# Kernel optimization log

Measured on AMD Instinct MI355X. Metric: run time of the kernel, lower is better.

The kernel has to match this reference:

```python
import jax, jax.numpy as jnp
import numpy as np

TOP_K = 8  # num_experts_per_tok
NEG_INF = -1e9


def setup_inputs() -> dict:
    key = jax.random.key(0)
    ks = jax.random.split(key, 6)
    B, S, H, I, E, G, GS = 1, 2048, 2048, 1408, 64, 8, 8
    sc = 0.02
    return {
        "hidden_states": jax.random.normal(ks[0], (B, S, H), jnp.float32),
        "gate_w": jax.random.normal(ks[1], (E, H), jnp.float32) * sc,
        "mask_up_w": jax.random.normal(ks[2], (G, H, GS), jnp.float32) * sc,
        "gate_proj_w": jax.random.normal(ks[3], (G, I, H), jnp.float32) * sc,
        "up_proj_w": jax.random.normal(ks[4], (G, I, H), jnp.float32) * sc,
        "down_proj_w": jax.random.normal(ks[5], (G, H, I), jnp.float32) * sc,
        "inv_map": jnp.arange(G * GS, dtype=jnp.int64).reshape(G, GS),
    }


def reference(hidden_states, gate_w, mask_up_w, gate_proj_w, up_proj_w, down_proj_w, inv_map):
    B, S, H = hidden_states.shape
    x = hidden_states.reshape(-1, H)  # [N, H]
    N = x.shape[0]
    E = gate_w.shape[0]

    # Gate: softmax scores -> top-k routing (DeepSeek-style MoEGate)
    scores = jax.nn.softmax(x @ gate_w.T, axis=-1)          # [N, E]
    topk_w, topk_idx = jax.lax.top_k(scores, TOP_K)         # [N, K]

    # Per-expert routing weight: w_e[t, e] = sum_k topk_w[t,k] * (topk_idx[t,k]==e)
    w_e = jnp.zeros((N, E), x.dtype).at[jnp.arange(N)[:, None], topk_idx].add(topk_w)

    # Gather group-local weights: flat[t, g, i] for sub-expert i of group g
    flat = w_e[:, inv_map]                                   # [N, G, GS]
    scalar = flat.sum(-1)                                    # [N, G]
    soft = jax.nn.softmax(jnp.where(flat == 0, NEG_INF, flat), axis=-1)  # [N, G, GS]

    # Mask injection: x' = x + mask_up_proj(soft)
    xg = x[:, None, :] + jnp.einsum('ngi,ghi->ngh', soft, mask_up_w)     # [N, G, H]

    # SwiGLU per group
    g = jnp.einsum('ngh,gih->ngi', xg, gate_proj_w)          # [N, G, I]
    u = jnp.einsum('ngh,gih->ngi', xg, up_proj_w)            # [N, G, I]
    a = jax.nn.silu(g) * u
    d = jnp.einsum('ngi,ghi->ngh', a, down_proj_w)           # [N, G, H]

    # scalar * output, accumulated over groups (scalar==0 rows contribute 0,
    # matching the original's zero-masked scatter)
    y = jnp.einsum('ng,ngh->nh', scalar, d)
    return y.reshape(B, S, H)
```

## Files before the change

kernel.cpp:

```cpp
#include <hip/hip_runtime.h>

#define N_TOK 2048
#define H_DIM 2048
#define I_DIM 1408
#define E_EXP 64
#define G_GRP 8
#define KTOT  (G_GRP * I_DIM)

typedef __bf16 bf16x8 __attribute__((ext_vector_type(8)));
typedef float f32x4 __attribute__((ext_vector_type(4)));

__device__ __forceinline__ unsigned short f2bf(float f) {
    unsigned int u = __builtin_bit_cast(unsigned int, f);
    u += 0x7fffu + ((u >> 16) & 1u);
    return (unsigned short)(u >> 16);
}

__device__ __forceinline__ float bf2f(unsigned short s) {
    return __builtin_bit_cast(float, (unsigned int)s << 16);
}

__device__ __forceinline__ void gl_lds16(const void* g, void* l) {
    __builtin_amdgcn_global_load_lds(
        (const __attribute__((address_space(1))) unsigned int*)g,
        (__attribute__((address_space(3))) unsigned int*)l, 16, 0, 0);
}

__device__ __forceinline__ bf16x8 lds_frag(const unsigned short* sm, int row, int c) {
    return *(const bf16x8*)&sm[(row * 8 + (c ^ (row & 7))) * 8];
}

__global__ __launch_bounds__(256) void k_transpose(const float* __restrict__ gw,
                                                   float* __restrict__ gwT) {
    int i = blockIdx.x * 256 + threadIdx.x;
    int h = i >> 6, e = i & 63;
    gwT[i] = gw[e * H_DIM + h];
}

__global__ __launch_bounds__(256) void k_cvt(const float* __restrict__ in,
                                             unsigned short* __restrict__ out, int n4) {
    int i = blockIdx.x * 256 + threadIdx.x;
    if (i >= n4) return;
    float4 v = ((const float4*)in)[i];
    ushort4 o;
    o.x = f2bf(v.x); o.y = f2bf(v.y); o.z = f2bf(v.z); o.w = f2bf(v.w);
    ((ushort4*)out)[i] = o;
}

__global__ __launch_bounds__(256) void k_cvt_wd(const float* __restrict__ in,
                                                unsigned short* __restrict__ out) {
    int idx = blockIdx.x * 256 + threadIdx.x;
    int i4 = idx % (I_DIM / 4);
    int h  = (idx / (I_DIM / 4)) & (H_DIM - 1);
    int g  = idx / ((I_DIM / 4) * H_DIM);
    float4 v = ((const float4*)(in + ((size_t)g * H_DIM + h) * I_DIM))[i4];
    ushort4 o;
    o.x = f2bf(v.x); o.y = f2bf(v.y); o.z = f2bf(v.z); o.w = f2bf(v.w);
    ((ushort4*)(out + ((size_t)h * G_GRP + g) * I_DIM))[i4] = o;
}

__global__ __launch_bounds__(512) void k_gating(const float* __restrict__ x,
                                                const float* __restrict__ gwT,
                                                float* __restrict__ soft,
                                                float* __restrict__ scal) {
    __shared__ double smAcc[8][8][64];
    int t = threadIdx.x, wid = t >> 6, lane = t & 63;
    int n0 = blockIdx.x * 8;

    double acc[8];
#pragma unroll
    for (int k = 0; k < 8; ++k) acc[k] = 0.0;
    int h0 = wid * 256;
    for (int h = h0; h < h0 + 256; ++h) {
        float gv = gwT[h * 64 + lane];
#pragma unroll
        for (int tok = 0; tok < 8; ++tok)
            acc[tok] += (double)x[(size_t)(n0 + tok) * H_DIM + h] * (double)gv;
    }
#pragma unroll
    for (int tok = 0; tok < 8; ++tok) smAcc[wid][tok][lane] = acc[tok];
    __syncthreads();

    double lg = 0.0;
#pragma unroll
    for (int w2 = 0; w2 < 8; ++w2) lg += smAcc[w2][wid][lane];
    float logit = (float)lg;

    float mx = logit;
#pragma unroll
    for (int d = 1; d < 64; d <<= 1) mx = fmaxf(mx, __shfl_xor(mx, d));
    float ex = expf(logit - mx);
    float sm = ex;
#pragma unroll
    for (int d = 1; d < 64; d <<= 1) sm += __shfl_xor(sm, d);
    float prob = ex / sm;

    float cur = prob, w = 0.0f;
#pragma unroll
    for (int it = 0; it < 8; ++it) {
        float m = cur;
#pragma unroll
        for (int d = 1; d < 64; d <<= 1) m = fmaxf(m, __shfl_xor(m, d));
        unsigned long long msk = __ballot(cur == m);
        int first = __ffsll(msk) - 1;
        if (lane == first) { w = prob; cur = -1.0f; }
    }
    float wf = w;

    float s8 = wf;
#pragma unroll
    for (int d = 1; d < 8; d <<= 1) s8 += __shfl_xor(s8, d);
    float v = (wf == 0.0f) ? -1000000000.0f : wf;
    float m8 = v;
#pragma unroll
    for (int d = 1; d < 8; d <<= 1) m8 = fmaxf(m8, __shfl_xor(m8, d));
    float e8 = expf(v - m8);
    float q8 = e8;
#pragma unroll
    for (int d = 1; d < 8; d <<= 1) q8 += __shfl_xor(q8, d);

    int n = n0 + wid;
    soft[(size_t)n * 64 + lane] = e8 / q8;
    if ((lane & 7) == 0) scal[(size_t)n * 8 + (lane >> 3)] = s8;
}

__global__ __launch_bounds__(256) void k_xg(const float* __restrict__ x,
                                            const float* __restrict__ muw,
                                            const float* __restrict__ soft,
                                            unsigned short* __restrict__ xg) {
    int g = blockIdx.z, h0 = blockIdx.y * 256, n0 = blockIdx.x * 128;
    __shared__ float smMu[8][256];
    __shared__ float smSf[128][8];
    int t = threadIdx.x;
    {
        const float* p = muw + ((size_t)g * H_DIM + h0 + t) * 8;
#pragma unroll
        for (int s = 0; s < 8; ++s) smMu[s][t] = p[s];
        int r = t >> 1, s4 = (t & 1) * 4;
        float4 sv = *(const float4*)&soft[(size_t)(n0 + r) * 64 + g * 8 + s4];
        smSf[r][s4 + 0] = sv.x; smSf[r][s4 + 1] = sv.y;
        smSf[r][s4 + 2] = sv.z; smSf[r][s4 + 3] = sv.w;
    }
    __syncthreads();
    const float* xp = x + (size_t)n0 * H_DIM + h0 + t;
    unsigned short* op = xg + ((size_t)g * N_TOK + n0) * H_DIM + h0 + t;
    for (int r = 0; r < 128; ++r) {
        float corr = 0.0f;
#pragma unroll
        for (int s = 0; s < 8; ++s) corr += smSf[r][s] * smMu[s][t];
        op[(size_t)r * H_DIM] = f2bf(xp[(size_t)r * H_DIM] + corr);
    }
}

template<bool IS_UP>
__global__ __launch_bounds__(256) void k_gemm1(const unsigned short* __restrict__ xg,
                                               const unsigned short* __restrict__ w,
                                               const float* __restrict__ scal,
                                               unsigned short* __restrict__ aB) {
    int f = blockIdx.x;
    int g = f & 7, r = f >> 3;
    int m0 = (r & 15) * 128, i0 = (r >> 4) * 128;
    __shared__ __align__(16) unsigned short smA[8192], smB[8192];
    __shared__ float smS[128];
    int t = threadIdx.x, wid = t >> 6, lane = t & 63;
    int r16 = lane & 15, quad = lane >> 4;
    int wm = wid >> 1, wn = wid & 1;

    if (IS_UP && t < 128) smS[t] = scal[(size_t)(m0 + t) * 8 + g];

    const unsigned short* A = xg + (size_t)g * N_TOK * H_DIM;
    const unsigned short* B = w  + (size_t)g * I_DIM * H_DIM;

    f32x4 zero = {0.f, 0.f, 0.f, 0.f};
    f32x4 acc[4][4];
#pragma unroll
    for (int mi = 0; mi < 4; ++mi)
#pragma unroll
        for (int ni = 0; ni < 4; ++ni) acc[mi][ni] = zero;

    for (int k0 = 0; k0 < H_DIM; k0 += 64) {
#pragma unroll
        for (int j = 0; j < 4; ++j) {
            int issue = wid * 4 + j;
            int s = issue * 64 + lane;
            int row = s >> 3;
            int c = (s & 7) ^ (row & 7);
            gl_lds16(A + (size_t)(m0 + row) * H_DIM + k0 + c * 8, &smA[issue * 512]);
            gl_lds16(B + (size_t)(i0 + row) * H_DIM + k0 + c * 8, &smB[issue * 512]);
        }
        __syncthreads();
#pragma unroll
        for (int kh = 0; kh < 2; ++kh) {
            int cc = kh * 4 + quad;
            bf16x8 af[4], bf_[4];
#pragma unroll
            for (int mi = 0; mi < 4; ++mi) af[mi]  = lds_frag(smA, wm * 64 + mi * 16 + r16, cc);
#pragma unroll
            for (int ni = 0; ni < 4; ++ni) bf_[ni] = lds_frag(smB, wn * 64 + ni * 16 + r16, cc);
#pragma unroll
            for (int mi = 0; mi < 4; ++mi)
#pragma unroll
                for (int ni = 0; ni < 4; ++ni)
                    acc[mi][ni] = __builtin_amdgcn_mfma_f32_16x16x32_bf16(af[mi], bf_[ni], acc[mi][ni], 0, 0, 0);
        }
        __syncthreads();
    }

#pragma unroll
    for (int mi = 0; mi < 4; ++mi)
#pragma unroll
        for (int ni = 0; ni < 4; ++ni)
#pragma unroll
            for (int rr = 0; rr < 4; ++rr) {
                int rl = wm * 64 + mi * 16 + quad * 4 + rr;
                int row = m0 + rl;
                int col = i0 + wn * 64 + ni * 16 + r16;
                size_t pos = ((size_t)row * G_GRP + g) * I_DIM + col;
                if (!IS_UP) {
                    aB[pos] = f2bf(acc[mi][ni][rr]);
                } else {
                    float gv = bf2f(aB[pos]);
                    float sv = gv / (1.0f + __expf(-gv));
                    aB[pos] = f2bf(sv * acc[mi][ni][rr] * smS[rl]);
                }
            }
}

__global__ __launch_bounds__(256) void k_gemm2(const unsigned short* __restrict__ aB,
                                               const unsigned short* __restrict__ wd,
                                               float* __restrict__ out) {
    int m0 = blockIdx.x * 128, h0 = blockIdx.y * 128;
    int kbase = blockIdx.z * (KTOT / 4);
    __shared__ __align__(16) unsigned short smA[8192], smB[8192];
    int t = threadIdx.x, wid = t >> 6, lane = t & 63;
    int r16 = lane & 15, quad = lane >> 4;
    int wm = wid >> 1, wn = wid & 1;

    f32x4 zero = {0.f, 0.f, 0.f, 0.f};
    f32x4 acc[4][4];
#pragma unroll
    for (int mi = 0; mi < 4; ++mi)
#pragma unroll
        for (int ni = 0; ni < 4; ++ni) acc[mi][ni] = zero;

    for (int k0 = kbase; k0 < kbase + KTOT / 4; k0 += 64) {
#pragma unroll
        for (int j = 0; j < 4; ++j) {
            int issue = wid * 4 + j;
            int s = issue * 64 + lane;
            int row = s >> 3;
            int c = (s & 7) ^ (row & 7);
            gl_lds16(aB + (size_t)(m0 + row) * KTOT + k0 + c * 8, &smA[issue * 512]);
            gl_lds16(wd + (size_t)(h0 + row) * KTOT + k0 + c * 8, &smB[issue * 512]);
        }
        __syncthreads();
#pragma unroll
        for (int kh = 0; kh < 2; ++kh) {
            int cc = kh * 4 + quad;
            bf16x8 af[4], bf_[4];
#pragma unroll
            for (int mi = 0; mi < 4; ++mi) af[mi]  = lds_frag(smA, wm * 64 + mi * 16 + r16, cc);
#pragma unroll
            for (int ni = 0; ni < 4; ++ni) bf_[ni] = lds_frag(smB, wn * 64 + ni * 16 + r16, cc);
#pragma unroll
            for (int mi = 0; mi < 4; ++mi)
#pragma unroll
                for (int ni = 0; ni < 4; ++ni)
                    acc[mi][ni] = __builtin_amdgcn_mfma_f32_16x16x32_bf16(af[mi], bf_[ni], acc[mi][ni], 0, 0, 0);
        }
        __syncthreads();
    }

#pragma unroll
    for (int mi = 0; mi < 4; ++mi)
#pragma unroll
        for (int ni = 0; ni < 4; ++ni)
#pragma unroll
            for (int rr = 0; rr < 4; ++rr) {
                int row = m0 + wm * 64 + mi * 16 + quad * 4 + rr;
                int col = h0 + wn * 64 + ni * 16 + r16;
                atomicAdd(&out[(size_t)row * H_DIM + col], acc[mi][ni][rr]);
            }
}

extern "C" void kernel_launch(void* const* d_in, const int* in_sizes, int n_in,
                              void* d_out, int out_size, void* d_ws, size_t ws_size,
                              hipStream_t stream) {
    const float* x   = (const float*)d_in[0];
    const float* gw  = (const float*)d_in[1];
    const float* mu  = (const float*)d_in[2];
    const float* wgp = (const float*)d_in[3];
    const float* wup = (const float*)d_in[4];
    const float* wdp = (const float*)d_in[5];
    float* out = (float*)d_out;
    char* ws = (char*)d_ws;

    float* gwT  = (float*)(ws + 0);
    float* soft = (float*)(ws + 524288);
    float* scal = (float*)(ws + 1048576);
    unsigned short* wgB = (unsigned short*)(ws + 1114112);
    unsigned short* wuB = (unsigned short*)(ws + 47251456);
    unsigned short* wdB = (unsigned short*)(ws + 93388800);
    unsigned short* xg  = (unsigned short*)(ws + 139526144);
    unsigned short* aB  = (unsigned short*)(ws + 206635008);

    hipMemsetAsync(d_out, 0, (size_t)N_TOK * H_DIM * sizeof(float), stream);
    k_transpose<<<512, 256, 0, stream>>>(gw, gwT);
    int n4 = G_GRP * I_DIM * H_DIM / 4;
    k_cvt<<<(n4 + 255) / 256, 256, 0, stream>>>(wgp, wgB, n4);
    k_cvt<<<(n4 + 255) / 256, 256, 0, stream>>>(wup, wuB, n4);
    k_cvt_wd<<<n4 / 256, 256, 0, stream>>>(wdp, wdB);
    k_gating<<<N_TOK / 8, 512, 0, stream>>>(x, gwT, soft, scal);
    k_xg<<<dim3(16, 8, 8), 256, 0, stream>>>(x, mu, soft, xg);
    k_gemm1<false><<<1408, 256, 0, stream>>>(xg, wgB, scal, aB);
    k_gemm1<true><<<1408, 256, 0, stream>>>(xg, wuB, scal, aB);
    k_gemm2<<<dim3(16, 16, 4), 256, 0, stream>>>(aB, wdB, out);
}
```

Before: 851.3 us.

## Fuse gate/up GEMMs, merge prep kernels, vectorize mask injection, halve GEMM2 split-K

Merges the transpose and three weight-conversion kernels into one prep launch. Fuses the gate and up projection GEMMs into one kernel that computes both accumulators per tile and applies SiLU, multiply and scale in the epilogue, so the gate intermediate no longer makes a bf16 round trip. The mask-injection kernel now keeps mask weights in registers and uses float4 loads with ushort4 stores. GEMM2 split-K drops from 4 to 2, which halves the atomic or accumulation traffic but also halves the grid size.

```diff
diff --git a/kernel.cpp b/kernel.cpp
--- a/kernel.cpp
+++ b/kernel.cpp
@@ -6,6 +6,8 @@
 #define E_EXP 64
 #define G_GRP 8
 #define KTOT  (G_GRP * I_DIM)
+#define NQ    (G_GRP * I_DIM * H_DIM / 4)
+#define NQB   (NQ / 256)
 
 typedef __bf16 bf16x8 __attribute__((ext_vector_type(8)));
 typedef float f32x4 __attribute__((ext_vector_type(4)));
@@ -16,10 +18,6 @@
     return (unsigned short)(u >> 16);
 }
 
-__device__ __forceinline__ float bf2f(unsigned short s) {
-    return __builtin_bit_cast(float, (unsigned int)s << 16);
-}
-
 __device__ __forceinline__ void gl_lds16(const void* g, void* l) {
     __builtin_amdgcn_global_load_lds(
         (const __attribute__((address_space(1))) unsigned int*)g,
@@ -30,33 +28,36 @@
     return *(const bf16x8*)&sm[(row * 8 + (c ^ (row & 7))) * 8];
 }
 
-__global__ __launch_bounds__(256) void k_transpose(const float* __restrict__ gw,
-                                                   float* __restrict__ gwT) {
-    int i = blockIdx.x * 256 + threadIdx.x;
-    int h = i >> 6, e = i & 63;
-    gwT[i] = gw[e * H_DIM + h];
-}
-
-__global__ __launch_bounds__(256) void k_cvt(const float* __restrict__ in,
-                                             unsigned short* __restrict__ out, int n4) {
-    int i = blockIdx.x * 256 + threadIdx.x;
-    if (i >= n4) return;
-    float4 v = ((const float4*)in)[i];
-    ushort4 o;
-    o.x = f2bf(v.x); o.y = f2bf(v.y); o.z = f2bf(v.z); o.w = f2bf(v.w);
-    ((ushort4*)out)[i] = o;
-}
-
-__global__ __launch_bounds__(256) void k_cvt_wd(const float* __restrict__ in,
-                                                unsigned short* __restrict__ out) {
-    int idx = blockIdx.x * 256 + threadIdx.x;
-    int i4 = idx % (I_DIM / 4);
-    int h  = (idx / (I_DIM / 4)) & (H_DIM - 1);
-    int g  = idx / ((I_DIM / 4) * H_DIM);
-    float4 v = ((const float4*)(in + ((size_t)g * H_DIM + h) * I_DIM))[i4];
-    ushort4 o;
-    o.x = f2bf(v.x); o.y = f2bf(v.y); o.z = f2bf(v.z); o.w = f2bf(v.w);
-    ((ushort4*)(out + ((size_t)h * G_GRP + g) * I_DIM))[i4] = o;
+__global__ __launch_bounds__(256) void k_prep(const float* __restrict__ gw,
+                                              const float* __restrict__ wgp,
+                                              const float* __restrict__ wup,
+                                              const float* __restrict__ wdp,
+                                              float* __restrict__ gwT,
+                                              unsigned short* __restrict__ wgB,
+                                              unsigned short* __restrict__ wuB,
+                                              unsigned short* __restrict__ wdB) {
+    int b = blockIdx.x, t = threadIdx.x;
+    if (b < 2 * NQB) {
+        const float* in = (b < NQB) ? wgp : wup;
+        unsigned short* out = (b < NQB) ? wgB : wuB;
+        int i = (b < NQB ? b : b - NQB) * 256 + t;
+        float4 v = ((const float4*)in)[i];
+        ushort4 o;
+        o.x = f2bf(v.x); o.y = f2bf(v.y); o.z = f2bf(v.z); o.w = f2bf(v.w);
+        ((ushort4*)out)[i] = o;
+    } else if (b < 3 * NQB) {
+        int idx = (b - 2 * NQB) * 256 + t;
+        int i4 = idx % (I_DIM / 4);
+        int h  = (idx / (I_DIM / 4)) & (H_DIM - 1);
+        int g  = idx / ((I_DIM / 4) * H_DIM);
+        float4 v = ((const float4*)(wdp + ((size_t)g * H_DIM + h) * I_DIM))[i4];
+        ushort4 o;
+        o.x = f2bf(v.x); o.y = f2bf(v.y); o.z = f2bf(v.z); o.w = f2bf(v.w);
+        ((ushort4*)(wdB + ((size_t)h * G_GRP + g) * I_DIM))[i4] = o;
+    } else {
+        int i = (b - 3 * NQB) * 256 + t;
+        gwT[i] = gw[(i & 63) * H_DIM + (i >> 6)];
+    }
 }
 
 __global__ __launch_bounds__(512) void k_gating(const float* __restrict__ x,
@@ -128,55 +129,69 @@
                                             const float* __restrict__ muw,
                                             const float* __restrict__ soft,
                                             unsigned short* __restrict__ xg) {
-    int g = blockIdx.z, h0 = blockIdx.y * 256, n0 = blockIdx.x * 128;
-    __shared__ float smMu[8][256];
+    int g = blockIdx.z, h0 = blockIdx.y * 1024, n0 = blockIdx.x * 128;
     __shared__ float smSf[128][8];
     int t = threadIdx.x;
     {
-        const float* p = muw + ((size_t)g * H_DIM + h0 + t) * 8;
-#pragma unroll
-        for (int s = 0; s < 8; ++s) smMu[s][t] = p[s];
         int r = t >> 1, s4 = (t & 1) * 4;
         float4 sv = *(const float4*)&soft[(size_t)(n0 + r) * 64 + g * 8 + s4];
         smSf[r][s4 + 0] = sv.x; smSf[r][s4 + 1] = sv.y;
         smSf[r][s4 + 2] = sv.z; smSf[r][s4 + 3] = sv.w;
     }
+    int hh = t * 4;
+    float mu[8][4];
+#pragma unroll
+    for (int j = 0; j < 4; ++j) {
+        const float4* p = (const float4*)(muw + ((size_t)g * H_DIM + h0 + hh + j) * 8);
+        float4 a = p[0], b = p[1];
+        mu[0][j] = a.x; mu[1][j] = a.y; mu[2][j] = a.z; mu[3][j] = a.w;
+        mu[4][j] = b.x; mu[5][j] = b.y; mu[6][j] = b.z; mu[7][j] = b.w;
+    }
     __syncthreads();
-    const float* xp = x + (size_t)n0 * H_DIM + h0 + t;
-    unsigned short* op = xg + ((size_t)g * N_TOK + n0) * H_DIM + h0 + t;
     for (int r = 0; r < 128; ++r) {
-        float corr = 0.0f;
-#pragma unroll
-        for (int s = 0; s < 8; ++s) corr += smSf[r][s] * smMu[s][t];
-        op[(size_t)r * H_DIM] = f2bf(xp[(size_t)r * H_DIM] + corr);
-    }
-}
-
-template<bool IS_UP>
+        float4 xv = *(const float4*)&x[(size_t)(n0 + r) * H_DIM + h0 + hh];
+        float c0 = xv.x, c1 = xv.y, c2 = xv.z, c3 = xv.w;
+#pragma unroll
+        for (int s = 0; s < 8; ++s) {
+            float w = smSf[r][s];
+            c0 += w * mu[s][0]; c1 += w * mu[s][1];
+            c2 += w * mu[s][2]; c3 += w * mu[s][3];
+        }
+        ushort4 o;
+        o.x = f2bf(c0); o.y = f2bf(c1); o.z = f2bf(c2); o.w = f2bf(c3);
+        *(ushort4*)&xg[((size_t)g * N_TOK + n0 + r) * H_DIM + h0 + hh] = o;
+    }
+}
+
 __global__ __launch_bounds__(256) void k_gemm1(const unsigned short* __restrict__ xg,
-                                               const unsigned short* __restrict__ w,
+                                               const unsigned short* __restrict__ wg,
+                                               const unsigned short* __restrict__ wu,
                                                const float* __restrict__ scal,
                                                unsigned short* __restrict__ aB) {
     int f = blockIdx.x;
     int g = f & 7, r = f >> 3;
-    int m0 = (r & 15) * 128, i0 = (r >> 4) * 128;
-    __shared__ __align__(16) unsigned short smA[8192], smB[8192];
+    int m0 = (r & 15) * 128;
+    int n0 = (r >> 4) * 64;
+    __shared__ __align__(16) unsigned short smA[8192];
+    __shared__ __align__(16) unsigned short smG[4096];
+    __shared__ __align__(16) unsigned short smU[4096];
     __shared__ float smS[128];
     int t = threadIdx.x, wid = t >> 6, lane = t & 63;
     int r16 = lane & 15, quad = lane >> 4;
     int wm = wid >> 1, wn = wid & 1;
 
-    if (IS_UP && t < 128) smS[t] = scal[(size_t)(m0 + t) * 8 + g];
-
-    const unsigned short* A = xg + (size_t)g * N_TOK * H_DIM;
-    const unsigned short* B = w  + (size_t)g * I_DIM * H_DIM;
+    if (t < 128) smS[t] = scal[(size_t)(m0 + t) * 8 + g];
+
+    const unsigned short* A  = xg + (size_t)g * N_TOK * H_DIM;
+    const unsigned short* Bg = wg + (size_t)g * I_DIM * H_DIM;
+    const unsigned short* Bu = wu + (size_t)g * I_DIM * H_DIM;
 
     f32x4 zero = {0.f, 0.f, 0.f, 0.f};
-    f32x4 acc[4][4];
+    f32x4 accg[4][2], accu[4][2];
 #pragma unroll
     for (int mi = 0; mi < 4; ++mi)
 #pragma unroll
-        for (int ni = 0; ni < 4; ++ni) acc[mi][ni] = zero;
+        for (int ni = 0; ni < 2; ++ni) { accg[mi][ni] = zero; accu[mi][ni] = zero; }
 
     for (int k0 = 0; k0 < H_DIM; k0 += 64) {
 #pragma unroll
@@ -186,22 +201,36 @@
             int row = s >> 3;
             int c = (s & 7) ^ (row & 7);
             gl_lds16(A + (size_t)(m0 + row) * H_DIM + k0 + c * 8, &smA[issue * 512]);
-            gl_lds16(B + (size_t)(i0 + row) * H_DIM + k0 + c * 8, &smB[issue * 512]);
+        }
+#pragma unroll
+        for (int j = 0; j < 2; ++j) {
+            int issue = wid * 2 + j;
+            int s = issue * 64 + lane;
+            int row = s >> 3;
+            int c = (s & 7) ^ (row & 7);
+            gl_lds16(Bg + (size_t)(n0 + row) * H_DIM + k0 + c * 8, &smG[issue * 512]);
+            gl_lds16(Bu + (size_t)(n0 + row) * H_DIM + k0 + c * 8, &smU[issue * 512]);
         }
         __syncthreads();
 #pragma unroll
         for (int kh = 0; kh < 2; ++kh) {
             int cc = kh * 4 + quad;
-            bf16x8 af[4], bf_[4];
-#pragma unroll
-            for (int mi = 0; mi < 4; ++mi) af[mi]  = lds_frag(smA, wm * 64 + mi * 16 + r16, cc);
-#pragma unroll
-            for (int ni = 0; ni < 4; ++ni) bf_[ni] = lds_frag(smB, wn * 64 + ni * 16 + r16, cc);
+            bf16x8 af[4], bgf[2], buf_[2];
+#pragma unroll
+            for (int mi = 0; mi < 4; ++mi) af[mi] = lds_frag(smA, wm * 64 + mi * 16 + r16, cc);
+#pragma unroll
+            for (int ni = 0; ni < 2; ++ni) {
+                int rw = wn * 32 + ni * 16 + r16;
+                bgf[ni] = lds_frag(smG, rw, cc);
+                buf_[ni] = lds_frag(smU, rw, cc);
+            }
 #pragma unroll
             for (int mi = 0; mi < 4; ++mi)
 #pragma unroll
-                for (int ni = 0; ni < 4; ++ni)
-                    acc[mi][ni] = __builtin_amdgcn_mfma_f32_16x16x32_bf16(af[mi], bf_[ni], acc[mi][ni], 0, 0, 0);
+                for (int ni = 0; ni < 2; ++ni) {
+                    accg[mi][ni] = __builtin_amdgcn_mfma_f32_16x16x32_bf16(af[mi], bgf[ni], accg[mi][ni], 0, 0, 0);
+                    accu[mi][ni] = __builtin_amdgcn_mfma_f32_16x16x32_bf16(af[mi], buf_[ni], accu[mi][ni], 0, 0, 0);
+                }
         }
         __syncthreads();
     }
@@ -209,20 +238,15 @@
 #pragma unroll
     for (int mi = 0; mi < 4; ++mi)
 #pragma unroll
-        for (int ni = 0; ni < 4; ++ni)
+        for (int ni = 0; ni < 2; ++ni)
 #pragma unroll
             for (int rr = 0; rr < 4; ++rr) {
                 int rl = wm * 64 + mi * 16 + quad * 4 + rr;
                 int row = m0 + rl;
-                int col = i0 + wn * 64 + ni * 16 + r16;
-                size_t pos = ((size_t)row * G_GRP + g) * I_DIM + col;
-                if (!IS_UP) {
-                    aB[pos] = f2bf(acc[mi][ni][rr]);
-                } else {
-                    float gv = bf2f(aB[pos]);
-                    float sv = gv / (1.0f + __expf(-gv));
-                    aB[pos] = f2bf(sv * acc[mi][ni][rr] * smS[rl]);
-                }
+                int col = n0 + wn * 32 + ni * 16 + r16;
+                float gv = accg[mi][ni][rr];
+                float sv = gv / (1.0f + __expf(-gv));
+                aB[((size_t)row * G_GRP + g) * I_DIM + col] = f2bf(sv * accu[mi][ni][rr] * smS[rl]);
             }
 }
 
@@ -230,7 +254,7 @@
                                                const unsigned short* __restrict__ wd,
                                                float* __restrict__ out) {
     int m0 = blockIdx.x * 128, h0 = blockIdx.y * 128;
-    int kbase = blockIdx.z * (KTOT / 4);
+    int kbase = blockIdx.z * (KTOT / 2);
     __shared__ __align__(16) unsigned short smA[8192], smB[8192];
     int t = threadIdx.x, wid = t >> 6, lane = t & 63;
     int r16 = lane & 15, quad = lane >> 4;
@@ -243,7 +267,7 @@
 #pragma unroll
         for (int ni = 0; ni < 4; ++ni) acc[mi][ni] = zero;
 
-    for (int k0 = kbase; k0 < kbase + KTOT / 4; k0 += 64) {
+    for (int k0 = kbase; k0 < kbase + KTOT / 2; k0 += 64) {
 #pragma unroll
         for (int j = 0; j < 4; ++j) {
             int issue = wid * 4 + j;
@@ -305,14 +329,9 @@
     unsigned short* aB  = (unsigned short*)(ws + 206635008);
 
     hipMemsetAsync(d_out, 0, (size_t)N_TOK * H_DIM * sizeof(float), stream);
-    k_transpose<<<512, 256, 0, stream>>>(gw, gwT);
-    int n4 = G_GRP * I_DIM * H_DIM / 4;
-    k_cvt<<<(n4 + 255) / 256, 256, 0, stream>>>(wgp, wgB, n4);
-    k_cvt<<<(n4 + 255) / 256, 256, 0, stream>>>(wup, wuB, n4);
-    k_cvt_wd<<<n4 / 256, 256, 0, stream>>>(wdp, wdB);
+    k_prep<<<3 * NQB + 512, 256, 0, stream>>>(gw, wgp, wup, wdp, gwT, wgB, wuB, wdB);
     k_gating<<<N_TOK / 8, 512, 0, stream>>>(x, gwT, soft, scal);
-    k_xg<<<dim3(16, 8, 8), 256, 0, stream>>>(x, mu, soft, xg);
-    k_gemm1<false><<<1408, 256, 0, stream>>>(xg, wgB, scal, aB);
-    k_gemm1<true><<<1408, 256, 0, stream>>>(xg, wuB, scal, aB);
-    k_gemm2<<<dim3(16, 16, 4), 256, 0, stream>>>(aB, wdB, out);
-}
+    k_xg<<<dim3(16, 2, 8), 256, 0, stream>>>(x, mu, soft, xg);
+    k_gemm1<<<2816, 256, 0, stream>>>(xg, wgB, wuB, scal, aB);
+    k_gemm2<<<dim3(16, 16, 2), 256, 0, stream>>>(aB, wdB, out);
+}
```

Result: faster. 824.6 us (-3.1%).
